# Kernel tuning notes

Measured on AMD Instinct MI355X. Metric: run time of the kernel, lower is better.

Reference implementation:

```python
import jax, jax.numpy as jnp
import numpy as np

N = 50000      # nodes
E = 800000     # edges (before self-loops)
IN = 128       # in_dim
HID = 64       # hidden_dim
HEADS = 4
OUT = 64       # out_dim
NEG_SLOPE = 0.2
EPS = 1e-16


def gat_conv(x, src, dst, W, att_src, att_dst, b, heads, out_ch, concat):
    """PyG GATConv (eval mode): gather -> attention -> segment softmax -> scatter."""
    n = x.shape[0]
    h = (x @ W).reshape(n, heads, out_ch)                 # [N,H,C]
    a_s = (h * att_src).sum(-1)                           # [N,H]
    a_d = (h * att_dst).sum(-1)                           # [N,H]
    alpha = jax.nn.leaky_relu(a_s[src] + a_d[dst], NEG_SLOPE)   # [E,H]
    amax = jax.ops.segment_max(alpha, dst, num_segments=n)      # stable softmax per dst
    alpha = jnp.exp(alpha - amax[dst])
    denom = jax.ops.segment_sum(alpha, dst, num_segments=n)
    alpha = alpha / (denom[dst] + EPS)
    msg = h[src] * alpha[:, :, None]                      # [E,H,C]
    out = jax.ops.segment_sum(msg, dst, num_segments=n)   # [N,H,C]
    out = out.reshape(n, heads * out_ch) if concat else out.mean(axis=1)
    return out + b


def setup_inputs() -> dict:
    key = jax.random.key(0)
    ks = jax.random.split(key, 16)
    lin = lambda k, fi, fo: jax.random.normal(k, (fi, fo), jnp.float32) / jnp.sqrt(fi)
    x = jax.random.normal(ks[0], (N, IN), jnp.float32)
    edge_index = jax.random.randint(ks[1], (2, E), 0, N, dtype=jnp.int32)
    return {
        "x": x,
        "edge_index": edge_index,
        "W1": lin(ks[2], IN, HEADS * HID),
        "att_src1": jax.random.normal(ks[3], (HEADS, HID)) * 0.1,
        "att_dst1": jax.random.normal(ks[4], (HEADS, HID)) * 0.1,
        "b1": jnp.zeros((HEADS * HID,), jnp.float32),
        "W2": lin(ks[5], HEADS * HID, OUT),
        "att_src2": jax.random.normal(ks[6], (1, OUT)) * 0.1,
        "att_dst2": jax.random.normal(ks[7], (1, OUT)) * 0.1,
        "b2": jnp.zeros((OUT,), jnp.float32),
        "dW1": lin(ks[8], OUT, HID),
        "db1": jnp.zeros((HID,), jnp.float32),
        "dW2": lin(ks[9], HID, IN),
        "db2": jnp.zeros((IN,), jnp.float32),
    }


def reference(x, edge_index, W1, att_src1, att_dst1, b1, W2, att_src2, att_dst2, b2,
              dW1, db1, dW2, db2):
    n = x.shape[0]
    loops = jnp.arange(n, dtype=edge_index.dtype)         # add_self_loops (PyG default)
    src = jnp.concatenate([edge_index[0], loops])
    dst = jnp.concatenate([edge_index[1], loops])
    # encode (dropout is identity in eval mode)
    h = jax.nn.elu(gat_conv(x, src, dst, W1, att_src1, att_dst1, b1, HEADS, HID, True))
    z = gat_conv(h, src, dst, W2, att_src2, att_dst2, b2, 1, OUT, False)
    # F.normalize(z, p=2, dim=-1)
    z = z / jnp.clip(jnp.linalg.norm(z, axis=-1, keepdims=True), 1e-12)
    # feat_decoder: Linear -> ELU -> Linear
    x_hat = jax.nn.elu(z @ dW1 + db1) @ dW2 + db2
    return (z, x_hat)
```

## Files before the change

kernel.cpp:

```cpp
#include <hip/hip_runtime.h>
#include <hip/hip_bf16.h>


#define IN_DIM   128
#define C1       256
#define HEADS    4
#define HID      64
#define OUT_DIM  64

typedef __attribute__((ext_vector_type(8))) short short8;
typedef __attribute__((ext_vector_type(4))) float f32x4;

__device__ __forceinline__ float lrelu(float x) { return x > 0.f ? x : 0.2f * x; }
__device__ __forceinline__ float elu1(float x)  { return x > 0.f ? x : (__expf(x) - 1.f); }
__device__ __forceinline__ float expc(float x)  { return __expf(fminf(x, 60.f)); }
__device__ __forceinline__ float bfu(unsigned int u) {
    union { unsigned int i; float f; } c; c.i = u << 16; return c.f;
}
__device__ __forceinline__ unsigned short pk(float f) {
    union { float f; unsigned int i; } c; c.f = f;
    return (unsigned short)((c.i + 0x7fffu + ((c.i >> 16) & 1u)) >> 16);
}

__global__ __launch_bounds__(256) void w1f_k(const float* __restrict__ W1,
                                             unsigned short* __restrict__ W1f)
{
    const int idx = blockIdx.x * 256 + threadIdx.x;
    if (idx >= 64 * 64) return;
    const int lane = idx & 63, e = idx >> 6;
    const int nt = e >> 2, kc = e & 3, q = lane >> 4, c = lane & 15;
    unsigned short tmp[8];
    #pragma unroll
    for (int j = 0; j < 8; ++j)
        tmp[j] = pk(W1[(kc * 32 + q * 8 + j) * 256 + nt * 16 + c]);
    ushort4* dst = (ushort4*)(W1f + (size_t)idx * 8);
    dst[0] = make_ushort4(tmp[0], tmp[1], tmp[2], tmp[3]);
    dst[1] = make_ushort4(tmp[4], tmp[5], tmp[6], tmp[7]);
}

__global__ __launch_bounds__(256) void w2f_k(const float* __restrict__ W2,
                                             unsigned short* __restrict__ W2f)
{
    const int idx = blockIdx.x * 256 + threadIdx.x;
    if (idx >= 32 * 64) return;
    const int lane = idx & 63, e = idx >> 6;
    const int nt = e >> 3, kc = e & 7, q = lane >> 4, c = lane & 15;
    unsigned short tmp[8];
    #pragma unroll
    for (int j = 0; j < 8; ++j)
        tmp[j] = pk(W2[(kc * 32 + q * 8 + j) * 64 + nt * 16 + c]);
    ushort4* dst = (ushort4*)(W2f + (size_t)idx * 8);
    dst[0] = make_ushort4(tmp[0], tmp[1], tmp[2], tmp[3]);
    dst[1] = make_ushort4(tmp[4], tmp[5], tmp[6], tmp[7]);
}

__global__ __launch_bounds__(256) void gemm1_k(
    const float* __restrict__ x, const unsigned short* __restrict__ W1f,
    const float* __restrict__ as1, const float* __restrict__ ad1,
    unsigned short* __restrict__ h1b, float* __restrict__ a_s1,
    float* __restrict__ a_d1, int N)
{
    __shared__ short lds[64 * 264];
    const int t = threadIdx.x, w = t >> 6, l = t & 63;
    const int q = l >> 4, c = l & 15;
    const int n0 = blockIdx.x * 64;
    for (int i = t; i < 64 * 32; i += 256) {
        const int r = i >> 5, k4 = (i & 31) * 4;
        const int rn = min(n0 + r, N - 1);
        const float4 v = *(const float4*)&x[(size_t)rn * IN_DIM + k4];
        *(ushort4*)&lds[r * 136 + k4] =
            make_ushort4(pk(v.x), pk(v.y), pk(v.z), pk(v.w));
    }
    __syncthreads();
    short8 afr[4];
    const int arow = 16 * w + c;
    #pragma unroll
    for (int kc = 0; kc < 4; ++kc)
        afr[kc] = *(const short8*)&lds[arow * 136 + kc * 32 + q * 8];
    f32x4 acc[16];
    #pragma unroll
    for (int nt = 0; nt < 16; ++nt) acc[nt] = (f32x4){0.f, 0.f, 0.f, 0.f};
    #pragma unroll
    for (int nt = 0; nt < 16; ++nt) {
        #pragma unroll
        for (int kc = 0; kc < 4; ++kc) {
            const short8 bfr =
                *(const short8*)(W1f + ((size_t)(nt * 4 + kc) * 64 + l) * 8);
            acc[nt] = __builtin_amdgcn_mfma_f32_16x16x32_bf16(afr[kc], bfr,
                                                              acc[nt], 0, 0, 0);
        }
    }
    #pragma unroll
    for (int h = 0; h < 4; ++h) {
        float vsr[4] = {0.f, 0.f, 0.f, 0.f}, vdr[4] = {0.f, 0.f, 0.f, 0.f};
        #pragma unroll
        for (int n4 = 0; n4 < 4; ++n4) {
            const int nt = h * 4 + n4;
            const float sa = as1[nt * 16 + c], da = ad1[nt * 16 + c];
            #pragma unroll
            for (int r = 0; r < 4; ++r) {
                vsr[r] += acc[nt][r] * sa;
                vdr[r] += acc[nt][r] * da;
            }
        }
        #pragma unroll
        for (int r = 0; r < 4; ++r) {
            #pragma unroll
            for (int off = 1; off < 16; off <<= 1) {
                vsr[r] += __shfl_xor(vsr[r], off, 64);
                vdr[r] += __shfl_xor(vdr[r], off, 64);
            }
            const int node = n0 + 16 * w + q * 4 + r;
            if (c == 0 && node < N) {
                a_s1[node * 4 + h] = vsr[r];
                a_d1[node * 4 + h] = vdr[r];
            }
        }
    }
    __syncthreads();
    #pragma unroll
    for (int nt = 0; nt < 16; ++nt)
        #pragma unroll
        for (int r = 0; r < 4; ++r)
            lds[(16 * w + q * 4 + r) * 264 + nt * 16 + c] = (short)pk(acc[nt][r]);
    __syncthreads();
    for (int i = t; i < 64 * 32; i += 256) {
        const int r = i >> 5, ch = (i & 31) * 8;
        const int node = n0 + r;
        if (node < N)
            *(short8*)&h1b[(size_t)node * C1 + ch] =
                *(const short8*)&lds[r * 264 + ch];
    }
}

__global__ void deg_k(const int* __restrict__ ei, int E, int Etot,
                      int* __restrict__ rowptr)
{
    const int e = blockIdx.x * blockDim.x + threadIdx.x;
    if (e >= Etot) return;
    const int d = (e < E) ? ei[E + e] : e - E;
    atomicAdd(&rowptr[1 + d], 1);
}

__device__ __forceinline__ int blk_incl_scan(int v, int t) {
    __shared__ int wsum[4];
    const int lane = t & 63, wid = t >> 6;
    int s = v;
    #pragma unroll
    for (int off = 1; off < 64; off <<= 1) {
        const int u = __shfl_up(s, off, 64);
        if (lane >= off) s += u;
    }
    if (lane == 63) wsum[wid] = s;
    __syncthreads();
    int add = 0;
    #pragma unroll
    for (int k = 0; k < 4; ++k) if (k < wid) add += wsum[k];
    __syncthreads();
    return s + add;
}

__global__ __launch_bounds__(256) void scanA_k(const int* __restrict__ rowptr,
                                               int* __restrict__ psum, int N)
{
    const int t = threadIdx.x;
    const int i = blockIdx.x * 256 + t;
    int v = (i < N) ? rowptr[1 + i] : 0;
    #pragma unroll
    for (int off = 1; off < 64; off <<= 1) v += __shfl_xor(v, off, 64);
    __shared__ int ws[4];
    if ((t & 63) == 0) ws[t >> 6] = v;
    __syncthreads();
    if (t == 0) psum[blockIdx.x] = ws[0] + ws[1] + ws[2] + ws[3];
}

__global__ __launch_bounds__(256) void scanB_k(int* __restrict__ psum, int SC)
{
    const int t = threadIdx.x;
    const int v = (t < SC) ? psum[t] : 0;
    const int inc = blk_incl_scan(v, t);
    if (t < SC) psum[t] = inc - v;
}

__global__ __launch_bounds__(256) void scanC_k(int* __restrict__ rowptr,
                                               int* __restrict__ cursor,
                                               const int* __restrict__ psum, int N)
{
    const int t = threadIdx.x;
    const int i = blockIdx.x * 256 + t;
    const int v = (i < N) ? rowptr[1 + i] : 0;
    const int inc = blk_incl_scan(v, t);
    const int base = psum[blockIdx.x];
    if (i < N) {
        rowptr[1 + i] = base + inc;
        cursor[i]     = base + inc - v;
    }
}

__global__ void fill_k(const int* __restrict__ ei, int E, int Etot,
                       int* __restrict__ cursor, int* __restrict__ col,
                       int* __restrict__ row)
{
    const int e = blockIdx.x * blockDim.x + threadIdx.x;
    if (e >= Etot) return;
    int s, d;
    if (e < E) { s = ei[e]; d = ei[E + e]; } else { s = d = e - E; }
    const int pos = atomicAdd(&cursor[d], 1);
    col[pos] = s;
    row[pos] = d;
}

__global__ void ew1_k(const int* __restrict__ col, const int* __restrict__ row,
                      const float* __restrict__ a_s1, const float* __restrict__ a_d1,
                      float* __restrict__ ew1, int Etot)
{
    const int p = blockIdx.x * blockDim.x + threadIdx.x;
    if (p >= Etot) return;
    const int s = col[p], d = row[p];
    const float4 sv = *(const float4*)&a_s1[s * 4];
    const float4 dv = *(const float4*)&a_d1[d * 4];
    float4 w;
    w.x = expc(lrelu(sv.x + dv.x));
    w.y = expc(lrelu(sv.y + dv.y));
    w.z = expc(lrelu(sv.z + dv.z));
    w.w = expc(lrelu(sv.w + dv.w));
    *(float4*)&ew1[(size_t)p * 4] = w;
}

__global__ void ew2_k(const int* __restrict__ col, const int* __restrict__ row,
                      const float* __restrict__ a_s2, const float* __restrict__ a_d2,
                      float* __restrict__ ew2, int Etot)
{
    const int p = blockIdx.x * blockDim.x + threadIdx.x;
    if (p >= Etot) return;
    ew2[p] = expc(lrelu(a_s2[col[p]] + a_d2[row[p]]));
}

__global__ __launch_bounds__(256) void agg1_k(
    const int* __restrict__ rowptr, const int* __restrict__ col,
    const float* __restrict__ ew1, const unsigned short* __restrict__ h1b,
    const float* __restrict__ b1, unsigned short* __restrict__ hxb, int N)
{
    const int t = threadIdx.x, w = t >> 6, l = t & 63;
    const int n = blockIdx.x * 4 + w;
    if (n >= N) return;
    const int beg = rowptr[n], end = rowptr[n + 1];
    const int head = l >> 4;
    float a0 = 0.f, a1 = 0.f, a2 = 0.f, a3 = 0.f, wsum = 0.f;
    for (int t0 = beg; t0 < end; t0 += 16) {
        const int m = min(16, end - t0);
        const int pe = t0 + (l & 15);
        const int   scol = (pe < end) ? col[pe] : 0;
        const float wst  = (pe < end) ? ew1[(size_t)pe * 4 + head] : 0.f;
        for (int j0 = 0; j0 < m; j0 += 8) {
            ushort4 hv[8]; float wu[8];
            #pragma unroll
            for (int u = 0; u < 8; ++u) {
                const int su = __shfl(scol, j0 + u, 64);
                wu[u] = __shfl(wst, (l & 48) + j0 + u, 64);
                hv[u] = *(const ushort4*)(h1b + (size_t)su * C1 + 4 * l);
            }
            #pragma unroll
            for (int u = 0; u < 8; ++u) {
                a0 = fmaf(bfu(hv[u].x), wu[u], a0);
                a1 = fmaf(bfu(hv[u].y), wu[u], a1);
                a2 = fmaf(bfu(hv[u].z), wu[u], a2);
                a3 = fmaf(bfu(hv[u].w), wu[u], a3);
                wsum += wu[u];
            }
        }
    }
    const float4 bb = *(const float4*)&b1[4 * l];
    const float inv = 1.f / (wsum + 1e-16f);
    ushort4 o;
    o.x = pk(elu1(a0 * inv + bb.x));
    o.y = pk(elu1(a1 * inv + bb.y));
    o.z = pk(elu1(a2 * inv + bb.z));
    o.w = pk(elu1(a3 * inv + bb.w));
    *(ushort4*)&hxb[(size_t)n * C1 + 4 * l] = o;
}

__global__ __launch_bounds__(256) void gemm2_k(
    const unsigned short* __restrict__ hxb, const unsigned short* __restrict__ W2f,
    const float* __restrict__ as2, const float* __restrict__ ad2,
    unsigned short* __restrict__ h2b, float* __restrict__ a_s2,
    float* __restrict__ a_d2, int N)
{
    __shared__ short lds[64 * 264];
    const int t = threadIdx.x, w = t >> 6, l = t & 63;
    const int q = l >> 4, c = l & 15;
    const int n0 = blockIdx.x * 64;
    for (int i = t; i < 64 * 32; i += 256) {
        const int r = i >> 5, ch = (i & 31) * 8;
        const int rn = min(n0 + r, N - 1);
        *(short8*)&lds[r * 264 + ch] =
            *(const short8*)&hxb[(size_t)rn * C1 + ch];
    }
    __syncthreads();
    short8 afr[8];
    const int arow = 16 * w + c;
    #pragma unroll
    for (int kc = 0; kc < 8; ++kc)
        afr[kc] = *(const short8*)&lds[arow * 264 + kc * 32 + q * 8];
    f32x4 acc[4];
    #pragma unroll
    for (int nt = 0; nt < 4; ++nt) acc[nt] = (f32x4){0.f, 0.f, 0.f, 0.f};
    #pragma unroll
    for (int nt = 0; nt < 4; ++nt) {
        #pragma unroll
        for (int kc = 0; kc < 8; ++kc) {
            const short8 bfr =
                *(const short8*)(W2f + ((size_t)(nt * 8 + kc) * 64 + l) * 8);
            acc[nt] = __builtin_amdgcn_mfma_f32_16x16x32_bf16(afr[kc], bfr,
                                                              acc[nt], 0, 0, 0);
        }
    }
    {
        float vsr[4] = {0.f, 0.f, 0.f, 0.f}, vdr[4] = {0.f, 0.f, 0.f, 0.f};
        #pragma unroll
        for (int nt = 0; nt < 4; ++nt) {
            const float sa = as2[nt * 16 + c], da = ad2[nt * 16 + c];
            #pragma unroll
            for (int r = 0; r < 4; ++r) {
                vsr[r] += acc[nt][r] * sa;
                vdr[r] += acc[nt][r] * da;
            }
        }
        #pragma unroll
        for (int r = 0; r < 4; ++r) {
            #pragma unroll
            for (int off = 1; off < 16; off <<= 1) {
                vsr[r] += __shfl_xor(vsr[r], off, 64);
                vdr[r] += __shfl_xor(vdr[r], off, 64);
            }
            const int node = n0 + 16 * w + q * 4 + r;
            if (c == 0 && node < N) {
                a_s2[node] = vsr[r];
                a_d2[node] = vdr[r];
            }
        }
    }
    __syncthreads();
    #pragma unroll
    for (int nt = 0; nt < 4; ++nt)
        #pragma unroll
        for (int r = 0; r < 4; ++r)
            lds[(16 * w + q * 4 + r) * 72 + nt * 16 + c] = (short)pk(acc[nt][r]);
    __syncthreads();
    for (int i = t; i < 64 * 8; i += 256) {
        const int r = i >> 3, ch = (i & 7) * 8;
        const int node = n0 + r;
        if (node < N)
            *(short8*)&h2b[(size_t)node * OUT_DIM + ch] =
                *(const short8*)&lds[r * 72 + ch];
    }
}

__global__ __launch_bounds__(256) void agg2_k(
    const int* __restrict__ rowptr, const int* __restrict__ col,
    const float* __restrict__ ew2, const unsigned short* __restrict__ h2b,
    const float* __restrict__ b2, float* __restrict__ zout, int N)
{
    const int t = threadIdx.x, w = t >> 6, l = t & 63;
    const int n = blockIdx.x * 4 + w;
    if (n >= N) return;
    const int beg = rowptr[n], end = rowptr[n + 1];
    const int half = l >> 5, c2 = l & 31;
    float a0 = 0.f, a1 = 0.f, wsum = 0.f;
    for (int t0 = beg; t0 < end; t0 += 64) {
        const int m = min(64, end - t0);
        const int p = t0 + l;
        const int   scol = (p < end) ? col[p] : 0;
        const float wv   = (p < end) ? ew2[p] : 0.f;
        const int pairs = (m + 1) >> 1;
        for (int j0 = 0; j0 < pairs; j0 += 8) {
            unsigned int hv[8]; float wu[8];
            #pragma unroll
            for (int u = 0; u < 8; ++u) {
                const int e = 2 * (j0 + u) + half;
                const int su = __shfl(scol, e, 64);
                wu[u] = __shfl(wv, e, 64);
                hv[u] = *(const unsigned int*)(h2b + (size_t)su * OUT_DIM + 2 * c2);
            }
            #pragma unroll
            for (int u = 0; u < 8; ++u) {
                a0 = fmaf(bfu(hv[u] & 0xffffu), wu[u], a0);
                a1 = fmaf(bfu(hv[u] >> 16), wu[u], a1);
                wsum += wu[u];
            }
        }
    }
    a0   += __shfl_xor(a0, 32, 64);
    a1   += __shfl_xor(a1, 32, 64);
    wsum += __shfl_xor(wsum, 32, 64);
    const float inv = 1.f / (wsum + 1e-16f);
    float z0 = a0 * inv + b2[2 * c2];
    float z1 = a1 * inv + b2[2 * c2 + 1];
    float sq = z0 * z0 + z1 * z1;
    #pragma unroll
    for (int off = 1; off < 32; off <<= 1) sq += __shfl_xor(sq, off, 64);
    const float rn = 1.f / fmaxf(sqrtf(sq), 1e-12f);
    if (l < 32) {
        float2 o; o.x = z0 * rn; o.y = z1 * rn;
        *(float2*)&zout[(size_t)n * OUT_DIM + 2 * c2] = o;
    }
}

__global__ __launch_bounds__(256) void dec_k(
    const float* __restrict__ z,
    const float* __restrict__ dW1, const float* __restrict__ db1,
    const float* __restrict__ dW2, const float* __restrict__ db2,
    float* __restrict__ xhat, int N)
{
    __shared__ float zs[32 * 64];
    __shared__ float ts[32 * 64];
    const int t = threadIdx.x;
    const int n0 = blockIdx.x * 32;
    for (int i = t; i < 32 * 64; i += 256) {
        const int nb_l = i >> 6, k = i & 63;
        const int n = min(n0 + nb_l, N - 1);
        zs[(nb_l >> 3) * 512 + k * 8 + (nb_l & 7)] = z[(size_t)n * OUT_DIM + k];
    }
    __syncthreads();
    const int w = t >> 6, l = t & 63;
    const float* zw = zs + w * 512;
    float* tw = ts + w * 512;
    float acc[8] = {0.f, 0.f, 0.f, 0.f, 0.f, 0.f, 0.f, 0.f};
    #pragma unroll 4
    for (int k = 0; k < 64; ++k) {
        const float wv = dW1[k * HID + l];
        const float4 xa = *(const float4*)&zw[k * 8];
        const float4 xb = *(const float4*)&zw[k * 8 + 4];
        acc[0] += xa.x * wv; acc[1] += xa.y * wv;
        acc[2] += xa.z * wv; acc[3] += xa.w * wv;
        acc[4] += xb.x * wv; acc[5] += xb.y * wv;
        acc[6] += xb.z * wv; acc[7] += xb.w * wv;
    }
    const float bb = db1[l];
    #pragma unroll
    for (int nb = 0; nb < 8; ++nb) tw[l * 8 + nb] = elu1(acc[nb] + bb);
    __syncthreads();
    float a0[8] = {0.f, 0.f, 0.f, 0.f, 0.f, 0.f, 0.f, 0.f};
    float a1[8] = {0.f, 0.f, 0.f, 0.f, 0.f, 0.f, 0.f, 0.f};
    #pragma unroll 2
    for (int k = 0; k < 64; ++k) {
        const float w0 = dW2[k * IN_DIM + l];
        const float w1 = dW2[k * IN_DIM + 64 + l];
        const float4 xa = *(const float4*)&tw[k * 8];
        const float4 xb = *(const float4*)&tw[k * 8 + 4];
        const float xv[8] = {xa.x, xa.y, xa.z, xa.w, xb.x, xb.y, xb.z, xb.w};
        #pragma unroll
        for (int nb = 0; nb < 8; ++nb) {
            a0[nb] += xv[nb] * w0;
            a1[nb] += xv[nb] * w1;
        }
    }
    const float bb0 = db2[l], bb1 = db2[64 + l];
    #pragma unroll
    for (int nb = 0; nb < 8; ++nb) {
        const int n = n0 + w * 8 + nb;
        if (n >= N) break;
        xhat[(size_t)n * IN_DIM + l]      = a0[nb] + bb0;
        xhat[(size_t)n * IN_DIM + 64 + l] = a1[nb] + bb1;
    }
}

extern "C" void kernel_launch(void* const* d_in, const int* in_sizes, int n_in,
                              void* d_out, int out_size, void* d_ws, size_t ws_size,
                              hipStream_t stream)
{
    const float* x   = (const float*)d_in[0];
    const int*   ei  = (const int*)d_in[1];
    const float* W1  = (const float*)d_in[2];
    const float* as1 = (const float*)d_in[3];
    const float* ad1 = (const float*)d_in[4];
    const float* b1  = (const float*)d_in[5];
    const float* W2  = (const float*)d_in[6];
    const float* as2 = (const float*)d_in[7];
    const float* ad2 = (const float*)d_in[8];
    const float* b2  = (const float*)d_in[9];
    const float* dW1 = (const float*)d_in[10];
    const float* db1 = (const float*)d_in[11];
    const float* dW2 = (const float*)d_in[12];
    const float* db2 = (const float*)d_in[13];

    const int N    = in_sizes[0] / IN_DIM;
    const int E    = in_sizes[1] / 2;
    const int Etot = E + N;

    float* ws = (float*)d_ws;
    unsigned short* hxb = (unsigned short*)ws;
    float* a_s1 = ws   + (size_t)N * C1;
    float* a_d1 = a_s1 + (size_t)N * HEADS;
    float* a_s2 = a_d1 + (size_t)N * HEADS;
    float* a_d2 = a_s2 + (size_t)N;
    float* ew1  = a_d2 + (size_t)N;
    float* ew2  = ew1  + (size_t)Etot * HEADS;
    unsigned short* h1b = (unsigned short*)(ew2 + (size_t)Etot);
    unsigned short* h2b = h1b + (size_t)N * C1;
    int* rowptr = (int*)(h2b + (size_t)N * OUT_DIM);
    int* cursor = rowptr + (N + 1);
    int* col    = cursor + N;
    int* row    = col    + Etot;
    int* psum   = row    + Etot;
    unsigned short* W1f = (unsigned short*)(psum + 256);
    unsigned short* W2f = W1f + 64 * 64 * 8;

    const size_t needed = ((size_t)N * 428 + 257 + (size_t)Etot * 7) * 4 + 98304;
    if (ws_size < needed) return;

    hipMemsetAsync(rowptr, 0, (size_t)(N + 1) * sizeof(int), stream);

    const int eblk = (Etot + 255) / 256;
    const int SC   = (N + 255) / 256;
    const int mblk = (N + 63) / 64;
    w1f_k  <<<16, 256, 0, stream>>>(W1, W1f);
    w2f_k  <<<8, 256, 0, stream>>>(W2, W2f);
    gemm1_k<<<mblk, 256, 0, stream>>>(x, W1f, as1, ad1, h1b, a_s1, a_d1, N);
    deg_k  <<<eblk, 256, 0, stream>>>(ei, E, Etot, rowptr);
    scanA_k<<<SC, 256, 0, stream>>>(rowptr, psum, N);
    scanB_k<<<1, 256, 0, stream>>>(psum, SC);
    scanC_k<<<SC, 256, 0, stream>>>(rowptr, cursor, psum, N);
    fill_k <<<eblk, 256, 0, stream>>>(ei, E, Etot, cursor, col, row);
    ew1_k  <<<eblk, 256, 0, stream>>>(col, row, a_s1, a_d1, ew1, Etot);
    agg1_k <<<(N + 3) / 4, 256, 0, stream>>>(rowptr, col, ew1, h1b, b1, hxb, N);
    gemm2_k<<<mblk, 256, 0, stream>>>(hxb, W2f, as2, ad2, h2b, a_s2, a_d2, N);
    ew2_k  <<<eblk, 256, 0, stream>>>(col, row, a_s2, a_d2, ew2, Etot);
    agg2_k <<<(N + 3) / 4, 256, 0, stream>>>(rowptr, col, ew2, h2b, b2,
                                             (float*)d_out, N);
    dec_k  <<<(N + 31) / 32, 256, 0, stream>>>((const float*)d_out, dW1, db1,
                                               dW2, db2,
                                               (float*)d_out + (size_t)N * OUT_DIM, N);
}
```

Baseline: 385.0 us.

## Aggregate raw inputs before layer-1 projection and fold edge weights into aggregation

Layer-1 attention logits are now computed from x through precomputed vectors W1·att (u_s/u_d), so the projection no longer has to run before aggregation. Aggregation now gathers 128-dim bf16 x rows per edge and builds a per-head 512-wide aggregate, which a new GEMM kernel then multiplies by W1 with bias and ELU fused in. The separate edge-weight kernels and the row array are removed, and the exp-lrelu weights are computed inline in both aggregation kernels. This halves per-edge gather bytes in layer 1 (128 vs 256 bf16) and drops the ew1/ew2 traffic. The cost is a 512-wide intermediate per node, four times the FMAs per gathered element, and an extra GEMM pass over it.

```diff
diff --git a/kernel.cpp b/kernel.cpp
--- a/kernel.cpp
+++ b/kernel.cpp
@@ -23,8 +23,27 @@
 }
 
 __global__ __launch_bounds__(256) void w1f_k(const float* __restrict__ W1,
-                                             unsigned short* __restrict__ W1f)
-{
+                                             const float* __restrict__ as1,
+                                             const float* __restrict__ ad1,
+                                             unsigned short* __restrict__ W1f,
+                                             float* __restrict__ u_s,
+                                             float* __restrict__ u_d)
+{
+    if (blockIdx.x == 16) {
+        for (int idx = threadIdx.x; idx < 512; idx += 256) {
+            const int h = idx >> 7, k = idx & 127;
+            float ss = 0.f, dd = 0.f;
+            #pragma unroll 4
+            for (int c = 0; c < 64; ++c) {
+                const float wv = W1[k * 256 + h * 64 + c];
+                ss += wv * as1[h * 64 + c];
+                dd += wv * ad1[h * 64 + c];
+            }
+            u_s[idx] = ss;
+            u_d[idx] = dd;
+        }
+        return;
+    }
     const int idx = blockIdx.x * 256 + threadIdx.x;
     if (idx >= 64 * 64) return;
     const int lane = idx & 63, e = idx >> 6;
@@ -54,82 +73,35 @@
     dst[1] = make_ushort4(tmp[4], tmp[5], tmp[6], tmp[7]);
 }
 
-__global__ __launch_bounds__(256) void gemm1_k(
-    const float* __restrict__ x, const unsigned short* __restrict__ W1f,
-    const float* __restrict__ as1, const float* __restrict__ ad1,
-    unsigned short* __restrict__ h1b, float* __restrict__ a_s1,
-    float* __restrict__ a_d1, int N)
-{
-    __shared__ short lds[64 * 264];
-    const int t = threadIdx.x, w = t >> 6, l = t & 63;
-    const int q = l >> 4, c = l & 15;
-    const int n0 = blockIdx.x * 64;
-    for (int i = t; i < 64 * 32; i += 256) {
-        const int r = i >> 5, k4 = (i & 31) * 4;
-        const int rn = min(n0 + r, N - 1);
-        const float4 v = *(const float4*)&x[(size_t)rn * IN_DIM + k4];
-        *(ushort4*)&lds[r * 136 + k4] =
-            make_ushort4(pk(v.x), pk(v.y), pk(v.z), pk(v.w));
-    }
-    __syncthreads();
-    short8 afr[4];
-    const int arow = 16 * w + c;
-    #pragma unroll
-    for (int kc = 0; kc < 4; ++kc)
-        afr[kc] = *(const short8*)&lds[arow * 136 + kc * 32 + q * 8];
-    f32x4 acc[16];
-    #pragma unroll
-    for (int nt = 0; nt < 16; ++nt) acc[nt] = (f32x4){0.f, 0.f, 0.f, 0.f};
-    #pragma unroll
-    for (int nt = 0; nt < 16; ++nt) {
-        #pragma unroll
-        for (int kc = 0; kc < 4; ++kc) {
-            const short8 bfr =
-                *(const short8*)(W1f + ((size_t)(nt * 4 + kc) * 64 + l) * 8);
-            acc[nt] = __builtin_amdgcn_mfma_f32_16x16x32_bf16(afr[kc], bfr,
-                                                              acc[nt], 0, 0, 0);
-        }
-    }
+__global__ __launch_bounds__(256) void xprep_k(
+    const float* __restrict__ x, const float* __restrict__ u_s,
+    const float* __restrict__ u_d, unsigned short* __restrict__ xb,
+    float* __restrict__ a_s1, float* __restrict__ a_d1, int N)
+{
+    __shared__ float us[512], ud[512];
+    const int t = threadIdx.x;
+    for (int i = t; i < 512; i += 256) { us[i] = u_s[i]; ud[i] = u_d[i]; }
+    __syncthreads();
+    const int w = t >> 6, l = t & 63;
+    const int n = blockIdx.x * 4 + w;
+    if (n >= N) return;
+    const float2 xv = *(const float2*)&x[(size_t)n * IN_DIM + 2 * l];
+    const unsigned int p2 =
+        (unsigned int)pk(xv.x) | ((unsigned int)pk(xv.y) << 16);
+    *(unsigned int*)&xb[(size_t)n * IN_DIM + 2 * l] = p2;
     #pragma unroll
     for (int h = 0; h < 4; ++h) {
-        float vsr[4] = {0.f, 0.f, 0.f, 0.f}, vdr[4] = {0.f, 0.f, 0.f, 0.f};
-        #pragma unroll
-        for (int n4 = 0; n4 < 4; ++n4) {
-            const int nt = h * 4 + n4;
-            const float sa = as1[nt * 16 + c], da = ad1[nt * 16 + c];
-            #pragma unroll
-            for (int r = 0; r < 4; ++r) {
-                vsr[r] += acc[nt][r] * sa;
-                vdr[r] += acc[nt][r] * da;
-            }
-        }
-        #pragma unroll
-        for (int r = 0; r < 4; ++r) {
-            #pragma unroll
-            for (int off = 1; off < 16; off <<= 1) {
-                vsr[r] += __shfl_xor(vsr[r], off, 64);
-                vdr[r] += __shfl_xor(vdr[r], off, 64);
-            }
-            const int node = n0 + 16 * w + q * 4 + r;
-            if (c == 0 && node < N) {
-                a_s1[node * 4 + h] = vsr[r];
-                a_d1[node * 4 + h] = vdr[r];
-            }
-        }
-    }
-    __syncthreads();
-    #pragma unroll
-    for (int nt = 0; nt < 16; ++nt)
-        #pragma unroll
-        for (int r = 0; r < 4; ++r)
-            lds[(16 * w + q * 4 + r) * 264 + nt * 16 + c] = (short)pk(acc[nt][r]);
-    __syncthreads();
-    for (int i = t; i < 64 * 32; i += 256) {
-        const int r = i >> 5, ch = (i & 31) * 8;
-        const int node = n0 + r;
-        if (node < N)
-            *(short8*)&h1b[(size_t)node * C1 + ch] =
-                *(const short8*)&lds[r * 264 + ch];
+        float ps = xv.x * us[h * 128 + 2 * l] + xv.y * us[h * 128 + 2 * l + 1];
+        float pd = xv.x * ud[h * 128 + 2 * l] + xv.y * ud[h * 128 + 2 * l + 1];
+        #pragma unroll
+        for (int off = 1; off < 64; off <<= 1) {
+            ps += __shfl_xor(ps, off, 64);
+            pd += __shfl_xor(pd, off, 64);
+        }
+        if (l == 0) {
+            a_s1[n * 4 + h] = ps;
+            a_d1[n * 4 + h] = pd;
+        }
     }
 }
 
@@ -198,8 +170,7 @@
 }
 
 __global__ void fill_k(const int* __restrict__ ei, int E, int Etot,
-                       int* __restrict__ cursor, int* __restrict__ col,
-                       int* __restrict__ row)
+                       int* __restrict__ cursor, int* __restrict__ col)
 {
     const int e = blockIdx.x * blockDim.x + threadIdx.x;
     if (e >= Etot) return;
@@ -207,77 +178,121 @@
     if (e < E) { s = ei[e]; d = ei[E + e]; } else { s = d = e - E; }
     const int pos = atomicAdd(&cursor[d], 1);
     col[pos] = s;
-    row[pos] = d;
-}
-
-__global__ void ew1_k(const int* __restrict__ col, const int* __restrict__ row,
-                      const float* __restrict__ a_s1, const float* __restrict__ a_d1,
-                      float* __restrict__ ew1, int Etot)
-{
-    const int p = blockIdx.x * blockDim.x + threadIdx.x;
-    if (p >= Etot) return;
-    const int s = col[p], d = row[p];
-    const float4 sv = *(const float4*)&a_s1[s * 4];
-    const float4 dv = *(const float4*)&a_d1[d * 4];
-    float4 w;
-    w.x = expc(lrelu(sv.x + dv.x));
-    w.y = expc(lrelu(sv.y + dv.y));
-    w.z = expc(lrelu(sv.z + dv.z));
-    w.w = expc(lrelu(sv.w + dv.w));
-    *(float4*)&ew1[(size_t)p * 4] = w;
-}
-
-__global__ void ew2_k(const int* __restrict__ col, const int* __restrict__ row,
-                      const float* __restrict__ a_s2, const float* __restrict__ a_d2,
-                      float* __restrict__ ew2, int Etot)
-{
-    const int p = blockIdx.x * blockDim.x + threadIdx.x;
-    if (p >= Etot) return;
-    ew2[p] = expc(lrelu(a_s2[col[p]] + a_d2[row[p]]));
-}
-
-__global__ __launch_bounds__(256) void agg1_k(
+}
+
+__global__ __launch_bounds__(256) void agg1x_k(
     const int* __restrict__ rowptr, const int* __restrict__ col,
-    const float* __restrict__ ew1, const unsigned short* __restrict__ h1b,
-    const float* __restrict__ b1, unsigned short* __restrict__ hxb, int N)
+    const float* __restrict__ a_s1, const float* __restrict__ a_d1,
+    const unsigned short* __restrict__ xb, unsigned short* __restrict__ xagg,
+    int N)
 {
     const int t = threadIdx.x, w = t >> 6, l = t & 63;
     const int n = blockIdx.x * 4 + w;
     if (n >= N) return;
     const int beg = rowptr[n], end = rowptr[n + 1];
-    const int head = l >> 4;
-    float a0 = 0.f, a1 = 0.f, a2 = 0.f, a3 = 0.f, wsum = 0.f;
+    const int head = l >> 4, e16 = l & 15;
+    const float dv = a_d1[n * 4 + head];
+    float acc[4][2] = {{0.f,0.f},{0.f,0.f},{0.f,0.f},{0.f,0.f}};
+    float wsum = 0.f;
     for (int t0 = beg; t0 < end; t0 += 16) {
         const int m = min(16, end - t0);
-        const int pe = t0 + (l & 15);
+        const int pe = t0 + e16;
         const int   scol = (pe < end) ? col[pe] : 0;
-        const float wst  = (pe < end) ? ew1[(size_t)pe * 4 + head] : 0.f;
+        const float sv   = (pe < end) ? a_s1[scol * 4 + head] : 0.f;
+        const float wst  = (pe < end) ? expc(lrelu(sv + dv)) : 0.f;
+        wsum += wst;
         for (int j0 = 0; j0 < m; j0 += 8) {
-            ushort4 hv[8]; float wu[8];
+            unsigned int hv[8];
             #pragma unroll
             for (int u = 0; u < 8; ++u) {
                 const int su = __shfl(scol, j0 + u, 64);
-                wu[u] = __shfl(wst, (l & 48) + j0 + u, 64);
-                hv[u] = *(const ushort4*)(h1b + (size_t)su * C1 + 4 * l);
+                hv[u] = *(const unsigned int*)(xb + (size_t)su * IN_DIM + 2 * l);
             }
             #pragma unroll
             for (int u = 0; u < 8; ++u) {
-                a0 = fmaf(bfu(hv[u].x), wu[u], a0);
-                a1 = fmaf(bfu(hv[u].y), wu[u], a1);
-                a2 = fmaf(bfu(hv[u].z), wu[u], a2);
-                a3 = fmaf(bfu(hv[u].w), wu[u], a3);
-                wsum += wu[u];
-            }
-        }
-    }
-    const float4 bb = *(const float4*)&b1[4 * l];
+                const float x0 = bfu(hv[u] & 0xffffu);
+                const float x1 = bfu(hv[u] >> 16);
+                #pragma unroll
+                for (int h = 0; h < 4; ++h) {
+                    const float ww = __shfl(wst, h * 16 + j0 + u, 64);
+                    acc[h][0] = fmaf(x0, ww, acc[h][0]);
+                    acc[h][1] = fmaf(x1, ww, acc[h][1]);
+                }
+            }
+        }
+    }
+    #pragma unroll
+    for (int off = 1; off < 16; off <<= 1) wsum += __shfl_xor(wsum, off, 64);
     const float inv = 1.f / (wsum + 1e-16f);
-    ushort4 o;
-    o.x = pk(elu1(a0 * inv + bb.x));
-    o.y = pk(elu1(a1 * inv + bb.y));
-    o.z = pk(elu1(a2 * inv + bb.z));
-    o.w = pk(elu1(a3 * inv + bb.w));
-    *(ushort4*)&hxb[(size_t)n * C1 + 4 * l] = o;
+    float ih[4];
+    #pragma unroll
+    for (int h = 0; h < 4; ++h) ih[h] = __shfl(inv, h * 16, 64);
+    #pragma unroll
+    for (int h = 0; h < 4; ++h) {
+        const unsigned int o =
+            (unsigned int)pk(acc[h][0] * ih[h]) |
+            ((unsigned int)pk(acc[h][1] * ih[h]) << 16);
+        *(unsigned int*)&xagg[(size_t)n * 512 + h * 128 + 2 * l] = o;
+    }
+}
+
+__global__ __launch_bounds__(256) void gemm1b_k(
+    const unsigned short* __restrict__ xagg, const unsigned short* __restrict__ W1f,
+    const float* __restrict__ b1, unsigned short* __restrict__ hxb, int N)
+{
+    __shared__ short lds[64 * 264];
+    const int t = threadIdx.x, w = t >> 6, l = t & 63;
+    const int q = l >> 4, c = l & 15;
+    const int n0 = blockIdx.x * 64;
+    const int arow = 16 * w + c;
+    f32x4 acc[16];
+    #pragma unroll
+    for (int nt = 0; nt < 16; ++nt) acc[nt] = (f32x4){0.f, 0.f, 0.f, 0.f};
+    #pragma unroll
+    for (int half = 0; half < 2; ++half) {
+        if (half) __syncthreads();
+        for (int i = t; i < 64 * 32; i += 256) {
+            const int r = i >> 5, ch = (i & 31) * 8;
+            const int rn = min(n0 + r, N - 1);
+            *(short8*)&lds[r * 264 + ch] =
+                *(const short8*)&xagg[(size_t)rn * 512 + half * 256 + ch];
+        }
+        __syncthreads();
+        #pragma unroll
+        for (int hh = 0; hh < 2; ++hh) {
+            const int h = half * 2 + hh;
+            short8 afr[4];
+            #pragma unroll
+            for (int kc = 0; kc < 4; ++kc)
+                afr[kc] = *(const short8*)&lds[arow * 264 + hh * 128 + kc * 32 + q * 8];
+            #pragma unroll
+            for (int nt = 0; nt < 4; ++nt) {
+                #pragma unroll
+                for (int kc = 0; kc < 4; ++kc) {
+                    const short8 bfr = *(const short8*)(W1f +
+                        ((size_t)((h * 4 + nt) * 4 + kc) * 64 + l) * 8);
+                    acc[h * 4 + nt] = __builtin_amdgcn_mfma_f32_16x16x32_bf16(
+                        afr[kc], bfr, acc[h * 4 + nt], 0, 0, 0);
+                }
+            }
+        }
+    }
+    __syncthreads();
+    #pragma unroll
+    for (int nt = 0; nt < 16; ++nt)
+        #pragma unroll
+        for (int r = 0; r < 4; ++r) {
+            const float v = elu1(acc[nt][r] + b1[nt * 16 + c]);
+            lds[(16 * w + q * 4 + r) * 264 + nt * 16 + c] = (short)pk(v);
+        }
+    __syncthreads();
+    for (int i = t; i < 64 * 32; i += 256) {
+        const int r = i >> 5, ch = (i & 31) * 8;
+        const int node = n0 + r;
+        if (node < N)
+            *(short8*)&hxb[(size_t)node * C1 + ch] =
+                *(const short8*)&lds[r * 264 + ch];
+    }
 }
 
 __global__ __launch_bounds__(256) void gemm2_k(
@@ -358,20 +373,22 @@
 
 __global__ __launch_bounds__(256) void agg2_k(
     const int* __restrict__ rowptr, const int* __restrict__ col,
-    const float* __restrict__ ew2, const unsigned short* __restrict__ h2b,
-    const float* __restrict__ b2, float* __restrict__ zout, int N)
+    const float* __restrict__ a_s2, const float* __restrict__ a_d2,
+    const unsigned short* __restrict__ h2b, const float* __restrict__ b2,
+    float* __restrict__ zout, int N)
 {
     const int t = threadIdx.x, w = t >> 6, l = t & 63;
     const int n = blockIdx.x * 4 + w;
     if (n >= N) return;
     const int beg = rowptr[n], end = rowptr[n + 1];
+    const float dn = a_d2[n];
     const int half = l >> 5, c2 = l & 31;
     float a0 = 0.f, a1 = 0.f, wsum = 0.f;
     for (int t0 = beg; t0 < end; t0 += 64) {
         const int m = min(64, end - t0);
         const int p = t0 + l;
         const int   scol = (p < end) ? col[p] : 0;
-        const float wv   = (p < end) ? ew2[p] : 0.f;
+        const float wv   = (p < end) ? expc(lrelu(a_s2[scol] + dn)) : 0.f;
         const int pairs = (m + 1) >> 1;
         for (int j0 = 0; j0 < pairs; j0 += 8) {
             unsigned int hv[8]; float wu[8];
@@ -488,47 +505,46 @@
     const int E    = in_sizes[1] / 2;
     const int Etot = E + N;
 
-    float* ws = (float*)d_ws;
-    unsigned short* hxb = (unsigned short*)ws;
-    float* a_s1 = ws   + (size_t)N * C1;
+    unsigned short* W1f = (unsigned short*)d_ws;
+    unsigned short* W2f = W1f + 32768;
+    float* u_s = (float*)(W2f + 16384);
+    float* u_d = u_s + 512;
+    unsigned short* hxb  = (unsigned short*)(u_d + 512);
+    unsigned short* xagg = hxb  + (size_t)N * C1;
+    unsigned short* xb   = xagg + (size_t)N * 512;
+    unsigned short* h2b  = xb   + (size_t)N * IN_DIM;
+    float* a_s1 = (float*)(h2b + (size_t)N * OUT_DIM);
     float* a_d1 = a_s1 + (size_t)N * HEADS;
     float* a_s2 = a_d1 + (size_t)N * HEADS;
     float* a_d2 = a_s2 + (size_t)N;
-    float* ew1  = a_d2 + (size_t)N;
-    float* ew2  = ew1  + (size_t)Etot * HEADS;
-    unsigned short* h1b = (unsigned short*)(ew2 + (size_t)Etot);
-    unsigned short* h2b = h1b + (size_t)N * C1;
-    int* rowptr = (int*)(h2b + (size_t)N * OUT_DIM);
+    int* rowptr = (int*)(a_d2 + (size_t)N);
     int* cursor = rowptr + (N + 1);
     int* col    = cursor + N;
-    int* row    = col    + Etot;
-    int* psum   = row    + Etot;
-    unsigned short* W1f = (unsigned short*)(psum + 256);
-    unsigned short* W2f = W1f + 64 * 64 * 8;
-
-    const size_t needed = ((size_t)N * 428 + 257 + (size_t)Etot * 7) * 4 + 98304;
+    int* psum   = col + Etot;
+
+    const size_t needed = (size_t)N * 1968 + (size_t)Etot * 4 + 103428;
     if (ws_size < needed) return;
 
     hipMemsetAsync(rowptr, 0, (size_t)(N + 1) * sizeof(int), stream);
 
-    const int eblk = (Etot + 255) / 256;
-    const int SC   = (N + 255) / 256;
-    const int mblk = (N + 63) / 64;
-    w1f_k  <<<16, 256, 0, stream>>>(W1, W1f);
-    w2f_k  <<<8, 256, 0, stream>>>(W2, W2f);
-    gemm1_k<<<mblk, 256, 0, stream>>>(x, W1f, as1, ad1, h1b, a_s1, a_d1, N);
-    deg_k  <<<eblk, 256, 0, stream>>>(ei, E, Etot, rowptr);
-    scanA_k<<<SC, 256, 0, stream>>>(rowptr, psum, N);
-    scanB_k<<<1, 256, 0, stream>>>(psum, SC);
-    scanC_k<<<SC, 256, 0, stream>>>(rowptr, cursor, psum, N);
-    fill_k <<<eblk, 256, 0, stream>>>(ei, E, Etot, cursor, col, row);
-    ew1_k  <<<eblk, 256, 0, stream>>>(col, row, a_s1, a_d1, ew1, Etot);
-    agg1_k <<<(N + 3) / 4, 256, 0, stream>>>(rowptr, col, ew1, h1b, b1, hxb, N);
-    gemm2_k<<<mblk, 256, 0, stream>>>(hxb, W2f, as2, ad2, h2b, a_s2, a_d2, N);
-    ew2_k  <<<eblk, 256, 0, stream>>>(col, row, a_s2, a_d2, ew2, Etot);
-    agg2_k <<<(N + 3) / 4, 256, 0, stream>>>(rowptr, col, ew2, h2b, b2,
-                                             (float*)d_out, N);
-    dec_k  <<<(N + 31) / 32, 256, 0, stream>>>((const float*)d_out, dW1, db1,
-                                               dW2, db2,
-                                               (float*)d_out + (size_t)N * OUT_DIM, N);
-}
+    const int eblk  = (Etot + 255) / 256;
+    const int SC    = (N + 255) / 256;
+    const int mblk  = (N + 63) / 64;
+    const int nblk4 = (N + 3) / 4;
+    w1f_k   <<<17, 256, 0, stream>>>(W1, as1, ad1, W1f, u_s, u_d);
+    w2f_k   <<<8, 256, 0, stream>>>(W2, W2f);
+    xprep_k <<<nblk4, 256, 0, stream>>>(x, u_s, u_d, xb, a_s1, a_d1, N);
+    deg_k   <<<eblk, 256, 0, stream>>>(ei, E, Etot, rowptr);
+    scanA_k <<<SC, 256, 0, stream>>>(rowptr, psum, N);
+    scanB_k <<<1, 256, 0, stream>>>(psum, SC);
+    scanC_k <<<SC, 256, 0, stream>>>(rowptr, cursor, psum, N);
+    fill_k  <<<eblk, 256, 0, stream>>>(ei, E, Etot, cursor, col);
+    agg1x_k <<<nblk4, 256, 0, stream>>>(rowptr, col, a_s1, a_d1, xb, xagg, N);
+    gemm1b_k<<<mblk, 256, 0, stream>>>(xagg, W1f, b1, hxb, N);
+    gemm2_k <<<mblk, 256, 0, stream>>>(hxb, W2f, as2, ad2, h2b, a_s2, a_d2, N);
+    agg2_k  <<<nblk4, 256, 0, stream>>>(rowptr, col, a_s2, a_d2, h2b, b2,
+                                        (float*)d_out, N);
+    dec_k   <<<(N + 31) / 32, 256, 0, stream>>>((const float*)d_out, dW1, db1,
+                                                dW2, db2,
+                                                (float*)d_out + (size_t)N * OUT_DIM, N);
+}
```

Result: no change. 391.4 us (+1.6%).
